# Kernel tuning notes

Measured on AMD Instinct MI355X. Metric: run time of the kernel, lower is better.

The kernel has to match this reference:

```python
import jax, jax.numpy as jnp
import numpy as np

N, E, IN_DIM, HID, HEADS = 50000, 400000, 128, 64, 4
NEG_SLOPE, LN_EPS = 0.2, 1e-5


def setup_inputs() -> dict:
    key = jax.random.key(0)
    ks = jax.random.split(key, 12)
    x = jax.random.normal(ks[0], (N, IN_DIM), dtype=jnp.float32)
    edge_index = jax.random.randint(ks[1], (2, E), 0, N, dtype=jnp.int64)
    s = 1.0 / np.sqrt(HID)
    return {
        "x": x,
        "edge_index": edge_index,
        "W_gcn": jax.random.normal(ks[2], (IN_DIM, HID), dtype=jnp.float32) / np.sqrt(IN_DIM),
        "b_gcn": jnp.zeros((HID,), dtype=jnp.float32),
        "W_gat": jax.random.normal(ks[3], (HID, HEADS * HID), dtype=jnp.float32) * s,
        "att_src": jax.random.normal(ks[4], (HEADS, HID), dtype=jnp.float32) * s,
        "att_dst": jax.random.normal(ks[5], (HEADS, HID), dtype=jnp.float32) * s,
        "b_gat": jnp.zeros((HID,), dtype=jnp.float32),
        "W_patch": jax.random.normal(ks[6], (HID, HID), dtype=jnp.float32) * s,
        "b_patch": jnp.zeros((HID,), dtype=jnp.float32),
        "gamma": jnp.ones((HID,), dtype=jnp.float32),
        "beta": jnp.zeros((HID,), dtype=jnp.float32),
    }


def _forward(x, edge_index, W_gcn, b_gcn, W_gat, att_src, att_dst, b_gat,
             W_patch, b_patch, gamma, beta):
    n = x.shape[0]
    loop = jnp.arange(n, dtype=edge_index.dtype)
    src = jnp.concatenate([edge_index[0], loop])  # self-loops appended (PyG default)
    dst = jnp.concatenate([edge_index[1], loop])

    # ---- GCNConv: symmetric degree normalization + scatter-add ----
    deg = jax.ops.segment_sum(jnp.ones_like(dst, dtype=jnp.float32), dst, num_segments=n)
    dinv = jnp.where(deg > 0, jax.lax.rsqrt(deg), 0.0)
    norm = dinv[src] * dinv[dst]  # [E+N]
    xw = x @ W_gcn  # [N,HID]
    h1 = jax.ops.segment_sum(xw[src] * norm[:, None], dst, num_segments=n) + b_gcn
    h1 = jax.nn.relu(h1)

    # ---- GATConv (heads=4, concat=False -> mean over heads) ----
    z = (h1 @ W_gat).reshape(n, HEADS, HID)  # [N,H,C]
    a_s = jnp.einsum('nhc,hc->nh', z, att_src)  # [N,H]
    a_d = jnp.einsum('nhc,hc->nh', z, att_dst)
    e = jax.nn.leaky_relu(a_s[src] + a_d[dst], negative_slope=NEG_SLOPE)  # [E+N,H]
    # segment-softmax over incoming edges per destination node
    m = jax.ops.segment_max(e, dst, num_segments=n)  # [N,H]
    ex = jnp.exp(e - m[dst])
    denom = jax.ops.segment_sum(ex, dst, num_segments=n)
    alpha = ex / denom[dst]  # [E+N,H]
    agg = jax.ops.segment_sum(z[src] * alpha[:, :, None], dst, num_segments=n)  # [N,H,C]
    h2 = jax.nn.relu(agg.mean(axis=1) + b_gat)

    # ---- residual fusion + LayerNorm (dropout is identity in eval) ----
    h_patch = h1 @ W_patch + b_patch
    h = h1 + h2 + h_patch
    mu = h.mean(axis=-1, keepdims=True)
    var = h.var(axis=-1, keepdims=True)
    return (h - mu) * jax.lax.rsqrt(var + LN_EPS) * gamma + beta


def reference(x, edge_index, W_gcn, b_gcn, W_gat, att_src, att_dst, b_gat,
              W_patch, b_patch, gamma, beta):
    return _forward(x, edge_index, W_gcn, b_gcn, W_gat, att_src, att_dst, b_gat,
                    W_patch, b_patch, gamma, beta)
```

## Files before the change

kernel.cpp:

```cpp
#include <hip/hip_runtime.h>
#include <math.h>

#define IN_DIM 128
#define HID 64
#define HEADS 4
#define NEG_SLOPE 0.2f
#define LN_EPS 1e-5f
#define APAD 328

typedef short bf16x8 __attribute__((ext_vector_type(8)));
typedef float f32x4  __attribute__((ext_vector_type(4)));
typedef unsigned short u16x4 __attribute__((ext_vector_type(4)));
typedef unsigned long long ull;

__device__ inline unsigned short f2bf(float f) {
    unsigned u = __float_as_uint(f);
    u += 0x7fffu + ((u >> 16) & 1u);
    return (unsigned short)(u >> 16);
}
__device__ inline float bf2f(unsigned short s) {
    return __uint_as_float(((unsigned)s) << 16);
}
__device__ inline float leaky(float v) { return v > 0.0f ? v : NEG_SLOPE * v; }

__global__ __launch_bounds__(256) void k_init(const void* ei, int E, int n,
                           int* flag, int* hist, ull* A,
                           const float* __restrict__ Wg, const float* __restrict__ Wp,
                           const float* __restrict__ Wgcn,
                           const float* __restrict__ att_s, const float* __restrict__ att_d,
                           unsigned short* __restrict__ Wt_post,
                           unsigned short* __restrict__ Wt_xw,
                           float* __restrict__ w_s, float* __restrict__ w_d) {
    int t = threadIdx.x;
    int role = blockIdx.x;
    if (role < 14) {
        int p = role * 256 + t;
        if (p < 2560) {
            int c = p & 63, kg = p >> 6;
            bf16x8 v;
#pragma unroll
            for (int j = 0; j < 8; j++) {
                int k = kg * 8 + j;
                float f;
                if (k < 256) f = 0.25f * Wg[(size_t)(k & 63) * 256 + (k >> 6) * 64 + c];
                else         f = Wp[(size_t)(k - 256) * 64 + c];
                v[j] = (short)f2bf(f);
            }
            *(bf16x8*)(&Wt_post[(size_t)p * 8]) = v;
        } else if (p < 2560 + 1024) {
            int q = p - 2560;
            int c = q & 63, kg = q >> 6;
            bf16x8 v;
#pragma unroll
            for (int j = 0; j < 8; j++)
                v[j] = (short)f2bf(Wgcn[(size_t)(kg * 8 + j) * 64 + c]);
            *(bf16x8*)(&Wt_xw[(size_t)q * 8]) = v;
        }
        return;
    }
    if (role == 14) {
        A[t] = 0ULL;
        __shared__ int s_bad;
        if (t == 0) s_bad = 0;
        __syncthreads();
        int lim = E < 512 ? E : 512;
        int bad = 0;
        for (int k = t; k < lim; k += 256)
            if (((const ull*)ei)[k] >= (ull)n) bad = 1;
        if (bad) s_bad = 1;
        __syncthreads();
        if (t == 0) *flag = s_bad ? 0 : 1;
        int h = t >> 6, k = t & 63;
        float ss = 0.0f, sd = 0.0f;
        for (int c = 0; c < HID; c++) {
            float w = Wg[(size_t)k * (HEADS * HID) + h * HID + c];
            ss += w * att_s[h * HID + c];
            sd += w * att_d[h * HID + c];
        }
        w_s[h * HID + k] = ss;
        w_d[h * HID + k] = sd;
        return;
    }
    __shared__ int s_bad2;
    if (t == 0) s_bad2 = 0;
    __syncthreads();
    int lim = E < 512 ? E : 512;
    int bad = 0;
    for (int k = t; k < lim; k += 256)
        if (((const ull*)ei)[k] >= (ull)n) bad = 1;
    if (bad) s_bad2 = 1;
    __syncthreads();
    int is64 = s_bad2 ? 0 : 1;
    int hb = role - 15;
    int nhb = gridDim.x - 15;
    for (int i = hb * 256 + t; i < E; i += nhb * 256) {
        int d;
        if (is64) d = (int)((const long long*)ei)[E + i];
        else      d = ((const int*)ei)[E + i];
        atomicAdd(&hist[d], 1);
    }
}

__global__ __launch_bounds__(256) void k_scan_lb(const int* __restrict__ hist,
                                                 ull* __restrict__ A,
                                                 int* __restrict__ row_ptr,
                                                 int* __restrict__ cursor,
                                                 float* __restrict__ dinv, int n) {
    __shared__ int s[256];
    __shared__ int sbase;
    int t = threadIdx.x, c = blockIdx.x;
    int w = t >> 6, lane = t & 63;
    int i = c * 256 + t;
    int v = (i < n) ? hist[i] : 0;
    s[t] = v;
    __syncthreads();
    for (int off = 1; off < 256; off <<= 1) {
        int xv = (t >= off) ? s[t - off] : 0;
        __syncthreads();
        s[t] += xv;
        __syncthreads();
    }
    int incl = s[t];
    int S = s[255];
    if (t == 0) {
        if (c == 0) { sbase = 0; atomicExch(&A[0], (2ULL << 32) | (unsigned)S); }
        else          atomicExch(&A[c], (1ULL << 32) | (unsigned)S);
    }
    if (c > 0 && w == 0) {
        long long run = 0;
        int p = c - 1;
        for (;;) {
            int idx = p - lane;
            unsigned st, val;
            if (idx >= 0) {
                ull v2 = atomicAdd(&A[idx], 0ULL);
                st = (unsigned)(v2 >> 32); val = (unsigned)v2;
            } else { st = 2u; val = 0u; }
            ull pm = __ballot(st == 2);
            ull zm = __ballot(st == 0);
            int firstP = pm ? (__ffsll((long long)pm) - 1) : 64;
            int firstZ = zm ? (__ffsll((long long)zm) - 1) : 64;
            if (firstZ < firstP) { __builtin_amdgcn_s_sleep(1); continue; }
            unsigned contrib = (lane <= firstP) ? val : 0u;
#pragma unroll
            for (int o = 1; o <= 32; o <<= 1) contrib += __shfl_xor(contrib, o, 64);
            run += contrib;
            if (firstP < 64) break;
            p -= 64;
        }
        if (lane == 0) {
            sbase = (int)run;
            atomicExch(&A[c], (2ULL << 32) | (unsigned)(run + (unsigned)S));
        }
    }
    __syncthreads();
    if (i < n) {
        int excl = sbase + incl - v;
        row_ptr[i] = excl;
        cursor[i] = excl;
        dinv[i] = rsqrtf((float)(v + 1));
    }
}

__global__ __launch_bounds__(256) void k_scatter_xw(const void* ei, int E,
                                                    const int* __restrict__ flag,
                                                    int* __restrict__ cursor,
                                                    int* __restrict__ col,
                                                    const float* __restrict__ x,
                                                    const unsigned short* __restrict__ Wt_g,
                                                    const float* __restrict__ dinv,
                                                    unsigned short* __restrict__ xws, int n) {
    __shared__ unsigned short Wt[16 * 64 * 8];
    int nsb = (E + 255) >> 8;
    if ((int)blockIdx.x < nsb) {
        int i = blockIdx.x * 256 + threadIdx.x;
        if (i >= E) return;
        int is64 = *flag;
        int s, d;
        if (is64) { s = (int)((const long long*)ei)[i]; d = (int)((const long long*)ei)[E + i]; }
        else      { s = ((const int*)ei)[i];            d = ((const int*)ei)[E + i]; }
        int pos = atomicAdd(&cursor[d], 1);
        col[pos] = s;
    } else {
        int bx = blockIdx.x - nsb;
        int t = threadIdx.x;
        for (int idx = t; idx < 1024; idx += 256)
            *(bf16x8*)(&Wt[idx * 8]) = *(const bf16x8*)(&Wt_g[(size_t)idx * 8]);
        __syncthreads();
        int lane = t & 63;
        int li = lane & 15, quad = lane >> 4;
        int w = t >> 6;
        int r0 = bx * 64 + w * 16;
        int rload = r0 + li; if (rload > n - 1) rload = n - 1;
        f32x4 acc[4];
#pragma unroll
        for (int i = 0; i < 4; i++) acc[i] = (f32x4){0.f, 0.f, 0.f, 0.f};
        const float* xp = x + (size_t)rload * IN_DIM + quad * 8;
#pragma unroll
        for (int ks = 0; ks < 4; ks++) {
            float4 p0 = *(const float4*)(xp + ks * 32);
            float4 p1 = *(const float4*)(xp + ks * 32 + 4);
            bf16x8 a;
            a[0] = (short)f2bf(p0.x); a[1] = (short)f2bf(p0.y);
            a[2] = (short)f2bf(p0.z); a[3] = (short)f2bf(p0.w);
            a[4] = (short)f2bf(p1.x); a[5] = (short)f2bf(p1.y);
            a[6] = (short)f2bf(p1.z); a[7] = (short)f2bf(p1.w);
            int kg = ks * 4 + quad;
#pragma unroll
            for (int tt = 0; tt < 4; tt++) {
                bf16x8 bfr = *(const bf16x8*)(&Wt[((kg * 64) + tt * 16 + li) * 8]);
                acc[tt] = __builtin_amdgcn_mfma_f32_16x16x32_bf16(a, bfr, acc[tt], 0, 0, 0);
            }
        }
#pragma unroll
        for (int reg = 0; reg < 4; reg++) {
            int r = r0 + quad * 4 + reg;
            if (r >= n) continue;
            float dv = dinv[r];
#pragma unroll
            for (int tt = 0; tt < 4; tt++)
                xws[(size_t)r * HID + tt * 16 + li] = f2bf(acc[tt][reg] * dv);
        }
    }
}

__global__ __launch_bounds__(256) void k_gcn(const int* __restrict__ col,
                                             const int* __restrict__ row_ptr,
                                             const int* __restrict__ hist,
                                             const float* __restrict__ dinv,
                                             const unsigned short* __restrict__ xws,
                                             const float* __restrict__ b,
                                             const float* __restrict__ w_s,
                                             const float* __restrict__ w_d,
                                             unsigned short* __restrict__ h1b,
                                             float4* __restrict__ a_s,
                                             float4* __restrict__ a_d, int n) {
    int t = threadIdx.x;
    int w = t >> 6, lane = t & 63, q = lane >> 4, li = lane & 15;
    int d = blockIdx.x * 4 + w;
    if (d >= n) return;
    int start = row_ptr[d], cnt = hist[d];
    float a0, a1, a2, a3;
    {
        u16x4 sv = *(const u16x4*)(xws + (size_t)d * HID + li * 4);
        float z = (q == 0) ? 1.0f : 0.0f;
        a0 = z * bf2f(sv[0]); a1 = z * bf2f(sv[1]);
        a2 = z * bf2f(sv[2]); a3 = z * bf2f(sv[3]);
    }
    for (int kb = q; kb < cnt; kb += 16) {
        int k1 = kb + 4, k2 = kb + 8, k3 = kb + 12;
        int i1 = k1 < cnt ? k1 : kb;
        int i2 = k2 < cnt ? k2 : kb;
        int i3 = k3 < cnt ? k3 : kb;
        int s0 = col[start + kb];
        int s1 = col[start + i1];
        int s2 = col[start + i2];
        int s3 = col[start + i3];
        u16x4 v0 = *(const u16x4*)(xws + (size_t)s0 * HID + li * 4);
        u16x4 v1 = *(const u16x4*)(xws + (size_t)s1 * HID + li * 4);
        u16x4 v2 = *(const u16x4*)(xws + (size_t)s2 * HID + li * 4);
        u16x4 v3 = *(const u16x4*)(xws + (size_t)s3 * HID + li * 4);
        float g1 = (k1 < cnt) ? 1.0f : 0.0f;
        float g2 = (k2 < cnt) ? 1.0f : 0.0f;
        float g3 = (k3 < cnt) ? 1.0f : 0.0f;
        a0 += (bf2f(v0[0]) + g1 * bf2f(v1[0])) + (g2 * bf2f(v2[0]) + g3 * bf2f(v3[0]));
        a1 += (bf2f(v0[1]) + g1 * bf2f(v1[1])) + (g2 * bf2f(v2[1]) + g3 * bf2f(v3[1]));
        a2 += (bf2f(v0[2]) + g1 * bf2f(v1[2])) + (g2 * bf2f(v2[2]) + g3 * bf2f(v3[2]));
        a3 += (bf2f(v0[3]) + g1 * bf2f(v1[3])) + (g2 * bf2f(v2[3]) + g3 * bf2f(v3[3]));
    }
    a0 += __shfl_xor(a0, 16, 64); a1 += __shfl_xor(a1, 16, 64);
    a2 += __shfl_xor(a2, 16, 64); a3 += __shfl_xor(a3, 16, 64);
    a0 += __shfl_xor(a0, 32, 64); a1 += __shfl_xor(a1, 32, 64);
    a2 += __shfl_xor(a2, 32, 64); a3 += __shfl_xor(a3, 32, 64);
    float dv = dinv[d];
    float4 bv = *(const float4*)(b + li * 4);
    float h0 = fmaxf(a0 * dv + bv.x, 0.0f);
    float h1 = fmaxf(a1 * dv + bv.y, 0.0f);
    float h2 = fmaxf(a2 * dv + bv.z, 0.0f);
    float h3 = fmaxf(a3 * dv + bv.w, 0.0f);
    if (q == 0) {
        u16x4 o;
        o[0] = f2bf(h0); o[1] = f2bf(h1); o[2] = f2bf(h2); o[3] = f2bf(h3);
        *(u16x4*)(h1b + (size_t)d * HID + li * 4) = o;
    }
    float4 u  = *(const float4*)(w_s + q * 64 + li * 4);
    float vs = h0 * u.x + h1 * u.y + h2 * u.z + h3 * u.w;
    float4 u2 = *(const float4*)(w_d + q * 64 + li * 4);
    float vd = h0 * u2.x + h1 * u2.y + h2 * u2.z + h3 * u2.w;
#pragma unroll
    for (int o = 1; o <= 8; o <<= 1) {
        vs += __shfl_xor(vs, o, 64);
        vd += __shfl_xor(vd, o, 64);
    }
    float vs1 = __shfl(vs, 16, 64), vs2 = __shfl(vs, 32, 64), vs3 = __shfl(vs, 48, 64);
    float vd1 = __shfl(vd, 16, 64), vd2 = __shfl(vd, 32, 64), vd3 = __shfl(vd, 48, 64);
    if (lane == 0) {
        a_s[d] = make_float4(vs, vs1, vs2, vs3);
        a_d[d] = make_float4(vd, vd1, vd2, vd3);
    }
}

__global__ __launch_bounds__(256) void k_attn_post(
        const int* __restrict__ col, const int* __restrict__ row_ptr,
        const int* __restrict__ hist,
        const float4* __restrict__ a_s, const float4* __restrict__ a_d,
        const unsigned short* __restrict__ h1b,
        const unsigned short* __restrict__ Wt_g,
        const float* __restrict__ bp, const float* __restrict__ bg,
        const float* __restrict__ gamma, const float* __restrict__ beta,
        float* __restrict__ out, int n) {
    __shared__ unsigned short Atile[16 * APAD];
    __shared__ float hbuf[16 * 68];
    int t = threadIdx.x;
    int w = t >> 6, lane = t & 63, q = lane >> 4, li = lane & 15;
    int rowbase = blockIdx.x * 16;

    for (int j = 0; j < 4; j++) {
        int r = w * 4 + j;
        int d = rowbase + r;
        if (d >= n) {
            for (int c = lane; c < 320; c += 64) Atile[r * APAD + c] = 0;
            continue;
        }
        int start = row_ptr[d], cnt = hist[d];
        float4 ad = a_d[d];
        float4 asd = a_s[d];
        u16x4 sv = *(const u16x4*)(h1b + (size_t)d * HID + li * 4);
        float e0 = __expf(leaky(asd.x + ad.x));
        float e1 = __expf(leaky(asd.y + ad.y));
        float e2 = __expf(leaky(asd.z + ad.z));
        float e3 = __expf(leaky(asd.w + ad.w));
        float z = (q == 0) ? 1.0f : 0.0f;
        float f0 = bf2f(sv[0]), f1 = bf2f(sv[1]), f2 = bf2f(sv[2]), f3 = bf2f(sv[3]);
        f32x4 A0 = {z * e0 * f0, z * e0 * f1, z * e0 * f2, z * e0 * f3};
        f32x4 A1 = {z * e1 * f0, z * e1 * f1, z * e1 * f2, z * e1 * f3};
        f32x4 A2 = {z * e2 * f0, z * e2 * f1, z * e2 * f2, z * e2 * f3};
        f32x4 A3 = {z * e3 * f0, z * e3 * f1, z * e3 * f2, z * e3 * f3};
        float l0 = z * e0, l1 = z * e1, l2 = z * e2, l3 = z * e3;
        for (int kb = q; kb < cnt; kb += 8) {
            int k1 = kb + 4;
            int i1 = k1 < cnt ? k1 : kb;
            int s0 = col[start + kb];
            int s1 = col[start + i1];
            float4 as0 = a_s[s0];
            float4 as1 = a_s[s1];
            u16x4 hv0 = *(const u16x4*)(h1b + (size_t)s0 * HID + li * 4);
            u16x4 hv1 = *(const u16x4*)(h1b + (size_t)s1 * HID + li * 4);
            float g1 = (k1 < cnt) ? 1.0f : 0.0f;
            float w00 = __expf(leaky(as0.x + ad.x));
            float w01 = __expf(leaky(as0.y + ad.y));
            float w02 = __expf(leaky(as0.z + ad.z));
            float w03 = __expf(leaky(as0.w + ad.w));
            float w10 = g1 * __expf(leaky(as1.x + ad.x));
            float w11 = g1 * __expf(leaky(as1.y + ad.y));
            float w12 = g1 * __expf(leaky(as1.z + ad.z));
            float w13 = g1 * __expf(leaky(as1.w + ad.w));
            float g00 = bf2f(hv0[0]), g01 = bf2f(hv0[1]);
            float g02 = bf2f(hv0[2]), g03 = bf2f(hv0[3]);
            float g10 = bf2f(hv1[0]), g11 = bf2f(hv1[1]);
            float g12 = bf2f(hv1[2]), g13 = bf2f(hv1[3]);
            A0[0] += w00 * g00 + w10 * g10; A0[1] += w00 * g01 + w10 * g11;
            A0[2] += w00 * g02 + w10 * g12; A0[3] += w00 * g03 + w10 * g13;
            A1[0] += w01 * g00 + w11 * g10; A1[1] += w01 * g01 + w11 * g11;
            A1[2] += w01 * g02 + w11 * g12; A1[3] += w01 * g03 + w11 * g13;
            A2[0] += w02 * g00 + w12 * g10; A2[1] += w02 * g01 + w12 * g11;
            A2[2] += w02 * g02 + w12 * g12; A2[3] += w02 * g03 + w12 * g13;
            A3[0] += w03 * g00 + w13 * g10; A3[1] += w03 * g01 + w13 * g11;
            A3[2] += w03 * g02 + w13 * g12; A3[3] += w03 * g03 + w13 * g13;
            l0 += w00 + w10; l1 += w01 + w11;
            l2 += w02 + w12; l3 += w03 + w13;
        }
#pragma unroll
        for (int c4 = 0; c4 < 4; c4++) {
            A0[c4] += __shfl_xor(A0[c4], 16, 64);
            A1[c4] += __shfl_xor(A1[c4], 16, 64);
            A2[c4] += __shfl_xor(A2[c4], 16, 64);
            A3[c4] += __shfl_xor(A3[c4], 16, 64);
        }
        l0 += __shfl_xor(l0, 16, 64); l1 += __shfl_xor(l1, 16, 64);
        l2 += __shfl_xor(l2, 16, 64); l3 += __shfl_xor(l3, 16, 64);
#pragma unroll
        for (int c4 = 0; c4 < 4; c4++) {
            A0[c4] += __shfl_xor(A0[c4], 32, 64);
            A1[c4] += __shfl_xor(A1[c4], 32, 64);
            A2[c4] += __shfl_xor(A2[c4], 32, 64);
            A3[c4] += __shfl_xor(A3[c4], 32, 64);
        }
        l0 += __shfl_xor(l0, 32, 64); l1 += __shfl_xor(l1, 32, 64);
        l2 += __shfl_xor(l2, 32, 64); l3 += __shfl_xor(l3, 32, 64);
        f32x4 Aq; float lq;
        if (q == 0)      { Aq = A0; lq = l0; }
        else if (q == 1) { Aq = A1; lq = l1; }
        else if (q == 2) { Aq = A2; lq = l2; }
        else             { Aq = A3; lq = l3; }
        float inv = 1.0f / lq;
        u16x4 o;
        o[0] = f2bf(Aq[0] * inv); o[1] = f2bf(Aq[1] * inv);
        o[2] = f2bf(Aq[2] * inv); o[3] = f2bf(Aq[3] * inv);
        *(u16x4*)(&Atile[r * APAD + q * 64 + li * 4]) = o;
        if (q == 0) *(u16x4*)(&Atile[r * APAD + 256 + li * 4]) = sv;
    }
    __syncthreads();

    f32x4 acc_a = {0.f, 0.f, 0.f, 0.f}, acc_h = {0.f, 0.f, 0.f, 0.f};
#pragma unroll
    for (int ks = 0; ks < 10; ks++) {
        int kg = ks * 4 + q;
        bf16x8 a = *(const bf16x8*)(&Atile[li * APAD + ks * 32 + q * 8]);
        bf16x8 bb = *(const bf16x8*)(&Wt_g[(size_t)(kg * 64 + w * 16 + li) * 8]);
        if (ks < 8) acc_a = __builtin_amdgcn_mfma_f32_16x16x32_bf16(a, bb, acc_a, 0, 0, 0);
        else        acc_h = __builtin_amdgcn_mfma_f32_16x16x32_bf16(a, bb, acc_h, 0, 0, 0);
    }
    int cc = w * 16 + li;
    float bgv = bg[cc], bpv = bp[cc];
#pragma unroll
    for (int reg = 0; reg < 4; reg++) {
        int r = q * 4 + reg;
        float h1c = bf2f(Atile[r * APAD + 256 + cc]);
        float h2v = fmaxf(acc_a[reg] + bgv, 0.0f);
        hbuf[r * 68 + cc] = h1c + h2v + acc_h[reg] + bpv;
    }
    __syncthreads();

    int row = t >> 4, lj = t & 15;
    f32x4 hv4 = *(const f32x4*)(&hbuf[row * 68 + lj * 4]);
    float s1 = (hv4[0] + hv4[1]) + (hv4[2] + hv4[3]);
    float s2 = (hv4[0] * hv4[0] + hv4[1] * hv4[1]) + (hv4[2] * hv4[2] + hv4[3] * hv4[3]);
#pragma unroll
    for (int o = 1; o <= 8; o <<= 1) {
        s1 += __shfl_xor(s1, o, 64);
        s2 += __shfl_xor(s2, o, 64);
    }
    float mu = s1 * (1.0f / 64.0f);
    float var = s2 * (1.0f / 64.0f) - mu * mu;
    float rs = rsqrtf(var + LN_EPS);
    int rg = rowbase + row;
    if (rg < n) {
        float4 g4 = *(const float4*)(gamma + lj * 4);
        float4 b4 = *(const float4*)(beta + lj * 4);
        float4 ov;
        ov.x = (hv4[0] - mu) * rs * g4.x + b4.x;
        ov.y = (hv4[1] - mu) * rs * g4.y + b4.y;
        ov.z = (hv4[2] - mu) * rs * g4.z + b4.z;
        ov.w = (hv4[3] - mu) * rs * g4.w + b4.w;
        *(float4*)(out + (size_t)rg * HID + lj * 4) = ov;
    }
}

extern "C" void kernel_launch(void* const* d_in, const int* in_sizes, int n_in,
                              void* d_out, int out_size, void* d_ws, size_t ws_size,
                              hipStream_t stream) {
    int n = in_sizes[0] / IN_DIM;
    int E = in_sizes[1] / 2;

    const float* x     = (const float*)d_in[0];
    const void*  ei    = d_in[1];
    const float* W_gcn = (const float*)d_in[2];
    const float* b_gcn = (const float*)d_in[3];
    const float* W_gat = (const float*)d_in[4];
    const float* att_s = (const float*)d_in[5];
    const float* att_d = (const float*)d_in[6];
    const float* b_gat = (const float*)d_in[7];
    const float* W_p   = (const float*)d_in[8];
    const float* b_p   = (const float*)d_in[9];
    const float* gamma = (const float*)d_in[10];
    const float* beta  = (const float*)d_in[11];

    int n128 = ((n + 127) / 128) * 128;
    int nch  = (n + 255) / 256;
    int nsb  = (E + 255) / 256;
    int nhb  = nsb < 1024 ? nsb : 1024;
    if (nhb < 1) nhb = 1;

    float* ws = (float*)d_ws;
    size_t off = 0;
    int*   flag    = (int*)(ws + off);  off += 4;
    int*   hist    = (int*)(ws + off);  off += n;
    int*   row_ptr = (int*)(ws + off);  off += n;
    int*   cursor  = (int*)(ws + off);  off += n;
    int*   colv    = (int*)(ws + off);  off += E;
    float* dinv    = ws + off;          off += n;
    float* w_s     = ws + off;          off += HEADS * HID;
    float* w_d     = ws + off;          off += HEADS * HID;
    off = (off + 1) & ~(size_t)1;
    ull*   A       = (ull*)(ws + off);  off += 512;
    off = (off + 3) & ~(size_t)3;
    unsigned short* Wt_post = (unsigned short*)(ws + off); off += 2560 * 8 / 2;
    unsigned short* Wt_xw   = (unsigned short*)(ws + off); off += 1024 * 8 / 2;
    unsigned short* xws = (unsigned short*)(ws + off); off += (size_t)n * HID / 2;
    off = (off + 3) & ~(size_t)3;
    unsigned short* h1b = (unsigned short*)(ws + off); off += (size_t)n128 * HID / 2;
    off = (off + 3) & ~(size_t)3;
    float4* a_sv   = (float4*)(ws + off); off += (size_t)n * 4;
    float4* a_dv   = (float4*)(ws + off); off += (size_t)n * 4;

    hipMemsetAsync(hist, 0, (size_t)n * sizeof(int), stream);
    k_init<<<15 + nhb, 256, 0, stream>>>(ei, E, n, flag, hist, A,
                                         W_gat, W_p, W_gcn, att_s, att_d,
                                         Wt_post, Wt_xw, w_s, w_d);

    k_scan_lb<<<nch, 256, 0, stream>>>(hist, A, row_ptr, cursor, dinv, n);

    k_scatter_xw<<<nsb + (n + 63) / 64, 256, 0, stream>>>(ei, E, flag, cursor,
                                                          colv, x, Wt_xw,
                                                          dinv, xws, n);

    k_gcn<<<(n + 3) / 4, 256, 0, stream>>>(colv, row_ptr, hist, dinv, xws, b_gcn,
                                           w_s, w_d, h1b, a_sv, a_dv, n);

    k_attn_post<<<(n + 15) / 16, 256, 0, stream>>>(colv, row_ptr, hist, a_sv, a_dv,
                                                   h1b, Wt_post, b_p, b_gat,
                                                   gamma, beta, (float*)d_out, n);
}
```

Measured before the change: 213.0 us.

## Compute GAT neighbor aggregation as block-level MFMA over staged edge tiles

For each 16-node block whose total in-degree fits in a fixed capacity, the kernel stages all incoming edges in shared memory. It builds a bf16 attention-weight matrix P (64 head-rows by edges) and a swizzled tile of gathered source features, then runs the weighted aggregation as bf16 MFMA matmuls instead of per-lane scalar FMAs with shuffle reductions. Softmax denominators are accumulated with shared-memory atomics, and blocks that exceed the capacity fall back to the original per-row loop. The cost is extra shared memory, which may reduce occupancy, plus strided LDS reads for the B fragments and bf16 rounding of the attention weights.

```diff
diff --git a/kernel.cpp b/kernel.cpp
--- a/kernel.cpp
+++ b/kernel.cpp
@@ -7,6 +7,10 @@
 #define NEG_SLOPE 0.2f
 #define LN_EPS 1e-5f
 #define APAD 328
+#define EC 176
+#define KMAXP 192
+#define PADB 72
+#define PADP 200
 
 typedef short bf16x8 __attribute__((ext_vector_type(8)));
 typedef float f32x4  __attribute__((ext_vector_type(4)));
@@ -309,96 +313,239 @@
         const float* __restrict__ bp, const float* __restrict__ bg,
         const float* __restrict__ gamma, const float* __restrict__ beta,
         float* __restrict__ out, int n) {
-    __shared__ unsigned short Atile[16 * APAD];
-    __shared__ float hbuf[16 * 68];
+    __shared__ __align__(16) unsigned short P[64 * PADP];
+    __shared__ __align__(16) unsigned short Bls[KMAXP * PADB];
+    __shared__ __align__(16) unsigned short Atile[16 * APAD];
+    __shared__ float l_sh[64];
+    __shared__ int sls[KMAXP];
+    __shared__ int sb[17];
+    __shared__ float4 sad[16];
+    float* hbuf = (float*)P;
+
     int t = threadIdx.x;
     int w = t >> 6, lane = t & 63, q = lane >> 4, li = lane & 15;
     int rowbase = blockIdx.x * 16;
 
-    for (int j = 0; j < 4; j++) {
-        int r = w * 4 + j;
-        int d = rowbase + r;
-        if (d >= n) {
-            for (int c = lane; c < 320; c += 64) Atile[r * APAD + c] = 0;
-            continue;
-        }
-        int start = row_ptr[d], cnt = hist[d];
-        float4 ad = a_d[d];
-        float4 asd = a_s[d];
-        u16x4 sv = *(const u16x4*)(h1b + (size_t)d * HID + li * 4);
-        float e0 = __expf(leaky(asd.x + ad.x));
-        float e1 = __expf(leaky(asd.y + ad.y));
-        float e2 = __expf(leaky(asd.z + ad.z));
-        float e3 = __expf(leaky(asd.w + ad.w));
-        float z = (q == 0) ? 1.0f : 0.0f;
-        float f0 = bf2f(sv[0]), f1 = bf2f(sv[1]), f2 = bf2f(sv[2]), f3 = bf2f(sv[3]);
-        f32x4 A0 = {z * e0 * f0, z * e0 * f1, z * e0 * f2, z * e0 * f3};
-        f32x4 A1 = {z * e1 * f0, z * e1 * f1, z * e1 * f2, z * e1 * f3};
-        f32x4 A2 = {z * e2 * f0, z * e2 * f1, z * e2 * f2, z * e2 * f3};
-        f32x4 A3 = {z * e3 * f0, z * e3 * f1, z * e3 * f2, z * e3 * f3};
-        float l0 = z * e0, l1 = z * e1, l2 = z * e2, l3 = z * e3;
-        for (int kb = q; kb < cnt; kb += 8) {
-            int k1 = kb + 4;
-            int i1 = k1 < cnt ? k1 : kb;
-            int s0 = col[start + kb];
-            int s1 = col[start + i1];
-            float4 as0 = a_s[s0];
-            float4 as1 = a_s[s1];
-            u16x4 hv0 = *(const u16x4*)(h1b + (size_t)s0 * HID + li * 4);
-            u16x4 hv1 = *(const u16x4*)(h1b + (size_t)s1 * HID + li * 4);
-            float g1 = (k1 < cnt) ? 1.0f : 0.0f;
-            float w00 = __expf(leaky(as0.x + ad.x));
-            float w01 = __expf(leaky(as0.y + ad.y));
-            float w02 = __expf(leaky(as0.z + ad.z));
-            float w03 = __expf(leaky(as0.w + ad.w));
-            float w10 = g1 * __expf(leaky(as1.x + ad.x));
-            float w11 = g1 * __expf(leaky(as1.y + ad.y));
-            float w12 = g1 * __expf(leaky(as1.z + ad.z));
-            float w13 = g1 * __expf(leaky(as1.w + ad.w));
-            float g00 = bf2f(hv0[0]), g01 = bf2f(hv0[1]);
-            float g02 = bf2f(hv0[2]), g03 = bf2f(hv0[3]);
-            float g10 = bf2f(hv1[0]), g11 = bf2f(hv1[1]);
-            float g12 = bf2f(hv1[2]), g13 = bf2f(hv1[3]);
-            A0[0] += w00 * g00 + w10 * g10; A0[1] += w00 * g01 + w10 * g11;
-            A0[2] += w00 * g02 + w10 * g12; A0[3] += w00 * g03 + w10 * g13;
-            A1[0] += w01 * g00 + w11 * g10; A1[1] += w01 * g01 + w11 * g11;
-            A1[2] += w01 * g02 + w11 * g12; A1[3] += w01 * g03 + w11 * g13;
-            A2[0] += w02 * g00 + w12 * g10; A2[1] += w02 * g01 + w12 * g11;
-            A2[2] += w02 * g02 + w12 * g12; A2[3] += w02 * g03 + w12 * g13;
-            A3[0] += w03 * g00 + w13 * g10; A3[1] += w03 * g01 + w13 * g11;
-            A3[2] += w03 * g02 + w13 * g12; A3[3] += w03 * g03 + w13 * g13;
-            l0 += w00 + w10; l1 += w01 + w11;
-            l2 += w02 + w12; l3 += w03 + w13;
-        }
-#pragma unroll
-        for (int c4 = 0; c4 < 4; c4++) {
-            A0[c4] += __shfl_xor(A0[c4], 16, 64);
-            A1[c4] += __shfl_xor(A1[c4], 16, 64);
-            A2[c4] += __shfl_xor(A2[c4], 16, 64);
-            A3[c4] += __shfl_xor(A3[c4], 16, 64);
-        }
-        l0 += __shfl_xor(l0, 16, 64); l1 += __shfl_xor(l1, 16, 64);
-        l2 += __shfl_xor(l2, 16, 64); l3 += __shfl_xor(l3, 16, 64);
-#pragma unroll
-        for (int c4 = 0; c4 < 4; c4++) {
-            A0[c4] += __shfl_xor(A0[c4], 32, 64);
-            A1[c4] += __shfl_xor(A1[c4], 32, 64);
-            A2[c4] += __shfl_xor(A2[c4], 32, 64);
-            A3[c4] += __shfl_xor(A3[c4], 32, 64);
-        }
-        l0 += __shfl_xor(l0, 32, 64); l1 += __shfl_xor(l1, 32, 64);
-        l2 += __shfl_xor(l2, 32, 64); l3 += __shfl_xor(l3, 32, 64);
-        f32x4 Aq; float lq;
-        if (q == 0)      { Aq = A0; lq = l0; }
-        else if (q == 1) { Aq = A1; lq = l1; }
-        else if (q == 2) { Aq = A2; lq = l2; }
-        else             { Aq = A3; lq = l3; }
-        float inv = 1.0f / lq;
-        u16x4 o;
-        o[0] = f2bf(Aq[0] * inv); o[1] = f2bf(Aq[1] * inv);
-        o[2] = f2bf(Aq[2] * inv); o[3] = f2bf(Aq[3] * inv);
-        *(u16x4*)(&Atile[r * APAD + q * 64 + li * 4]) = o;
-        if (q == 0) *(u16x4*)(&Atile[r * APAD + 256 + li * 4]) = sv;
+    if (t < 17) {
+        int d2 = rowbase + t;
+        int dd = d2 < n ? d2 : n - 1;
+        sb[t] = row_ptr[dd] + ((d2 < n) ? 0 : hist[dd]);
+    }
+    if (t < 16) {
+        int d = rowbase + t;
+        sad[t] = (d < n) ? a_d[d] : make_float4(0.f, 0.f, 0.f, 0.f);
+    }
+    if (t < 64) l_sh[t] = 0.0f;
+    __syncthreads();
+    int start0 = sb[0];
+    int totc = sb[16] - start0;
+    int K_used = totc + 16;
+    int K_pad = (K_used + 31) & ~31;
+    bool fast = (totc <= EC);
+
+    if (fast) {
+        bf16x8 z8 = {0, 0, 0, 0, 0, 0, 0, 0};
+        for (int i = t; i < 64 * PADP / 8; i += 256) ((bf16x8*)P)[i] = z8;
+        for (int i = K_used * (PADB / 8) + t; i < K_pad * (PADB / 8); i += 256)
+            ((bf16x8*)Bls)[i] = z8;
+        if (t < totc) {
+            int e = t;
+            int s = col[start0 + e];
+            int j = 0;
+#pragma unroll
+            for (int jj = 1; jj < 16; jj++) j += (e >= (sb[jj] - start0)) ? 1 : 0;
+            float4 as = a_s[s], ad = sad[j];
+            unsigned short q0 = f2bf(__expf(leaky(as.x + ad.x)));
+            unsigned short q1 = f2bf(__expf(leaky(as.y + ad.y)));
+            unsigned short q2 = f2bf(__expf(leaky(as.z + ad.z)));
+            unsigned short q3 = f2bf(__expf(leaky(as.w + ad.w)));
+            P[(j * 4 + 0) * PADP + e] = q0;
+            P[(j * 4 + 1) * PADP + e] = q1;
+            P[(j * 4 + 2) * PADP + e] = q2;
+            P[(j * 4 + 3) * PADP + e] = q3;
+            sls[e] = s;
+            atomicAdd(&l_sh[j * 4 + 0], bf2f(q0));
+            atomicAdd(&l_sh[j * 4 + 1], bf2f(q1));
+            atomicAdd(&l_sh[j * 4 + 2], bf2f(q2));
+            atomicAdd(&l_sh[j * 4 + 3], bf2f(q3));
+        }
+        if (t < 16) {
+            int d = rowbase + t;
+            if (d < n) {
+                float4 as = a_s[d], ad = sad[t];
+                unsigned short q0 = f2bf(__expf(leaky(as.x + ad.x)));
+                unsigned short q1 = f2bf(__expf(leaky(as.y + ad.y)));
+                unsigned short q2 = f2bf(__expf(leaky(as.z + ad.z)));
+                unsigned short q3 = f2bf(__expf(leaky(as.w + ad.w)));
+                int e = totc + t;
+                P[(t * 4 + 0) * PADP + e] = q0;
+                P[(t * 4 + 1) * PADP + e] = q1;
+                P[(t * 4 + 2) * PADP + e] = q2;
+                P[(t * 4 + 3) * PADP + e] = q3;
+                sls[e] = d;
+                atomicAdd(&l_sh[t * 4 + 0], bf2f(q0));
+                atomicAdd(&l_sh[t * 4 + 1], bf2f(q1));
+                atomicAdd(&l_sh[t * 4 + 2], bf2f(q2));
+                atomicAdd(&l_sh[t * 4 + 3], bf2f(q3));
+            } else {
+                sls[totc + t] = 0;
+            }
+        }
+    }
+    __syncthreads();
+
+    if (fast) {
+        for (int idx = t; idx < K_used * 8; idx += 256) {
+            int e = idx >> 3, p = idx & 7;
+            int s = sls[e];
+            bf16x8 v = *(const bf16x8*)(h1b + (size_t)s * HID + p * 8);
+            int cb = p ^ ((e >> 3) & 3);
+            *(bf16x8*)(&Bls[e * PADB + cb * 8]) = v;
+        }
+        if (t < 128) {
+            int dl = t >> 3, p = t & 7;
+            int d = rowbase + dl;
+            bf16x8 v = {0, 0, 0, 0, 0, 0, 0, 0};
+            if (d < n) v = *(const bf16x8*)(h1b + (size_t)d * HID + p * 8);
+            *(bf16x8*)(&Atile[dl * APAD + 256 + p * 8]) = v;
+        }
+    }
+    __syncthreads();
+
+    if (fast) {
+        int rt0 = (w >> 1) * 2, ct0 = (w & 1) * 2;
+        f32x4 acc[2][2];
+#pragma unroll
+        for (int i = 0; i < 2; i++)
+#pragma unroll
+            for (int jj = 0; jj < 2; jj++) acc[i][jj] = (f32x4){0.f, 0.f, 0.f, 0.f};
+        int kmax = K_pad >> 5;
+        for (int ks = 0; ks < kmax; ks++) {
+            bf16x8 af0 = *(const bf16x8*)(&P[((rt0 + 0) * 16 + li) * PADP + ks * 32 + q * 8]);
+            bf16x8 af1 = *(const bf16x8*)(&P[((rt0 + 1) * 16 + li) * PADP + ks * 32 + q * 8]);
+            int kbase = ks * 32 + q * 8;
+            bf16x8 bf[2];
+#pragma unroll
+            for (int jj = 0; jj < 2; jj++) {
+                int c = (ct0 + jj) * 16 + li;
+                int ccol = (((c >> 3) ^ q) << 3) | (c & 7);
+                bf16x8 bb;
+#pragma unroll
+                for (int jx = 0; jx < 8; jx++)
+                    bb[jx] = (short)Bls[(kbase + jx) * PADB + ccol];
+                bf[jj] = bb;
+            }
+            acc[0][0] = __builtin_amdgcn_mfma_f32_16x16x32_bf16(af0, bf[0], acc[0][0], 0, 0, 0);
+            acc[0][1] = __builtin_amdgcn_mfma_f32_16x16x32_bf16(af0, bf[1], acc[0][1], 0, 0, 0);
+            acc[1][0] = __builtin_amdgcn_mfma_f32_16x16x32_bf16(af1, bf[0], acc[1][0], 0, 0, 0);
+            acc[1][1] = __builtin_amdgcn_mfma_f32_16x16x32_bf16(af1, bf[1], acc[1][1], 0, 0, 0);
+        }
+#pragma unroll
+        for (int i = 0; i < 2; i++) {
+            float invl[4];
+#pragma unroll
+            for (int reg = 0; reg < 4; reg++) {
+                int r = (rt0 + i) * 16 + q * 4 + reg;
+                float lv = l_sh[r];
+                invl[reg] = (lv > 0.0f) ? 1.0f / lv : 0.0f;
+            }
+#pragma unroll
+            for (int jj = 0; jj < 2; jj++) {
+                int c = (ct0 + jj) * 16 + li;
+#pragma unroll
+                for (int reg = 0; reg < 4; reg++) {
+                    int r = (rt0 + i) * 16 + q * 4 + reg;
+                    int dl = r >> 2, h = r & 3;
+                    Atile[dl * APAD + h * 64 + c] = f2bf(acc[i][jj][reg] * invl[reg]);
+                }
+            }
+        }
+    } else {
+        for (int j = 0; j < 4; j++) {
+            int r = w * 4 + j;
+            int d = rowbase + r;
+            if (d >= n) {
+                for (int c = lane; c < 320; c += 64) Atile[r * APAD + c] = 0;
+                continue;
+            }
+            int start = row_ptr[d], cnt = hist[d];
+            float4 ad = a_d[d];
+            float4 asd = a_s[d];
+            u16x4 sv = *(const u16x4*)(h1b + (size_t)d * HID + li * 4);
+            float e0 = __expf(leaky(asd.x + ad.x));
+            float e1 = __expf(leaky(asd.y + ad.y));
+            float e2 = __expf(leaky(asd.z + ad.z));
+            float e3 = __expf(leaky(asd.w + ad.w));
+            float z = (q == 0) ? 1.0f : 0.0f;
+            float f0 = bf2f(sv[0]), f1 = bf2f(sv[1]), f2 = bf2f(sv[2]), f3 = bf2f(sv[3]);
+            f32x4 A0 = {z * e0 * f0, z * e0 * f1, z * e0 * f2, z * e0 * f3};
+            f32x4 A1 = {z * e1 * f0, z * e1 * f1, z * e1 * f2, z * e1 * f3};
+            f32x4 A2 = {z * e2 * f0, z * e2 * f1, z * e2 * f2, z * e2 * f3};
+            f32x4 A3 = {z * e3 * f0, z * e3 * f1, z * e3 * f2, z * e3 * f3};
+            float l0 = z * e0, l1 = z * e1, l2 = z * e2, l3 = z * e3;
+            for (int kb = q; kb < cnt; kb += 8) {
+                int k1 = kb + 4;
+                int i1 = k1 < cnt ? k1 : kb;
+                int s0 = col[start + kb];
+                int s1 = col[start + i1];
+                float4 as0 = a_s[s0];
+                float4 as1 = a_s[s1];
+                u16x4 hv0 = *(const u16x4*)(h1b + (size_t)s0 * HID + li * 4);
+                u16x4 hv1 = *(const u16x4*)(h1b + (size_t)s1 * HID + li * 4);
+                float g1 = (k1 < cnt) ? 1.0f : 0.0f;
+                float w00 = __expf(leaky(as0.x + ad.x));
+                float w01 = __expf(leaky(as0.y + ad.y));
+                float w02 = __expf(leaky(as0.z + ad.z));
+                float w03 = __expf(leaky(as0.w + ad.w));
+                float w10 = g1 * __expf(leaky(as1.x + ad.x));
+                float w11 = g1 * __expf(leaky(as1.y + ad.y));
+                float w12 = g1 * __expf(leaky(as1.z + ad.z));
+                float w13 = g1 * __expf(leaky(as1.w + ad.w));
+                float g00 = bf2f(hv0[0]), g01 = bf2f(hv0[1]);
+                float g02 = bf2f(hv0[2]), g03 = bf2f(hv0[3]);
+                float g10 = bf2f(hv1[0]), g11 = bf2f(hv1[1]);
+                float g12 = bf2f(hv1[2]), g13 = bf2f(hv1[3]);
+                A0[0] += w00 * g00 + w10 * g10; A0[1] += w00 * g01 + w10 * g11;
+                A0[2] += w00 * g02 + w10 * g12; A0[3] += w00 * g03 + w10 * g13;
+                A1[0] += w01 * g00 + w11 * g10; A1[1] += w01 * g01 + w11 * g11;
+                A1[2] += w01 * g02 + w11 * g12; A1[3] += w01 * g03 + w11 * g13;
+                A2[0] += w02 * g00 + w12 * g10; A2[1] += w02 * g01 + w12 * g11;
+                A2[2] += w02 * g02 + w12 * g12; A2[3] += w02 * g03 + w12 * g13;
+                A3[0] += w03 * g00 + w13 * g10; A3[1] += w03 * g01 + w13 * g11;
+                A3[2] += w03 * g02 + w13 * g12; A3[3] += w03 * g03 + w13 * g13;
+                l0 += w00 + w10; l1 += w01 + w11;
+                l2 += w02 + w12; l3 += w03 + w13;
+            }
+#pragma unroll
+            for (int c4 = 0; c4 < 4; c4++) {
+                A0[c4] += __shfl_xor(A0[c4], 16, 64);
+                A1[c4] += __shfl_xor(A1[c4], 16, 64);
+                A2[c4] += __shfl_xor(A2[c4], 16, 64);
+                A3[c4] += __shfl_xor(A3[c4], 16, 64);
+            }
+            l0 += __shfl_xor(l0, 16, 64); l1 += __shfl_xor(l1, 16, 64);
+            l2 += __shfl_xor(l2, 16, 64); l3 += __shfl_xor(l3, 16, 64);
+#pragma unroll
+            for (int c4 = 0; c4 < 4; c4++) {
+                A0[c4] += __shfl_xor(A0[c4], 32, 64);
+                A1[c4] += __shfl_xor(A1[c4], 32, 64);
+                A2[c4] += __shfl_xor(A2[c4], 32, 64);
+                A3[c4] += __shfl_xor(A3[c4], 32, 64);
+            }
+            l0 += __shfl_xor(l0, 32, 64); l1 += __shfl_xor(l1, 32, 64);
+            l2 += __shfl_xor(l2, 32, 64); l3 += __shfl_xor(l3, 32, 64);
+            f32x4 Aq; float lq;
+            if (q == 0)      { Aq = A0; lq = l0; }
+            else if (q == 1) { Aq = A1; lq = l1; }
+            else if (q == 2) { Aq = A2; lq = l2; }
+            else             { Aq = A3; lq = l3; }
+            float inv = 1.0f / lq;
+            u16x4 o;
+            o[0] = f2bf(Aq[0] * inv); o[1] = f2bf(Aq[1] * inv);
+            o[2] = f2bf(Aq[2] * inv); o[3] = f2bf(Aq[3] * inv);
+            *(u16x4*)(&Atile[r * APAD + q * 64 + li * 4]) = o;
+            if (q == 0) *(u16x4*)(&Atile[r * APAD + 256 + li * 4]) = sv;
+        }
     }
     __syncthreads();
 
```

New measurement: 227.1 us. +6.6%, slower.
